# Performance work log

Hardware: AMD Instinct MI355X
Metric: run time of the kernel (lower is better)

Reference implementation:

```python
import jax, jax.numpy as jnp
import numpy as np

GRID = 480  # grid extent for both x and y voxel indices


def setup_inputs() -> dict:
    key = jax.random.key(0)
    k = jax.random.split(key, 8)
    B, N, FD, H1, H2, D = 4, 100000, 3, 128, 256, 64
    scale = 0.05
    pt_fea = jax.random.normal(k[0], (B, N, FD), dtype=jnp.float32)
    xy_ind = jax.random.randint(k[1], (B, N, 2), 0, GRID, dtype=jnp.int32)
    W1 = jax.random.normal(k[2], (FD, H1), dtype=jnp.float32) * scale
    b1 = jnp.zeros((H1,), dtype=jnp.float32)
    W2 = jax.random.normal(k[3], (H1, H2), dtype=jnp.float32) * scale
    b2 = jnp.zeros((H2,), dtype=jnp.float32)
    W3 = jax.random.normal(k[4], (H2, D), dtype=jnp.float32) * scale
    b3 = jnp.zeros((D,), dtype=jnp.float32)
    return {"pt_fea": pt_fea, "xy_ind": xy_ind, "W1": W1, "b1": b1,
            "W2": W2, "b2": b2, "W3": W3, "b3": b3}


def reference(pt_fea, xy_ind, W1, b1, W2, b2, W3, b3):
    B, N, FD = pt_fea.shape
    flat = pt_fea.reshape(B * N, FD)
    # pad xy_ind with batch id -> (b, x, y) per point
    bidx = jnp.repeat(jnp.arange(B, dtype=xy_ind.dtype), N)
    xy = xy_ind.reshape(B * N, 2)
    # lexicographic linear encoding so sorted linear order == torch.unique(dim=0) row order
    lin = (bidx.astype(jnp.int32) * GRID + xy[:, 0]) * GRID + xy[:, 1]
    unq_lin, unq_inv = jnp.unique(lin, return_inverse=True)
    M = int(unq_lin.shape[0])  # concrete: indices are concrete (eager unique)
    unq = jnp.stack([unq_lin // (GRID * GRID),
                     (unq_lin // GRID) % GRID,
                     unq_lin % GRID], axis=1)
    # per-point MLP: 3 -> 128 -> 256 -> 64
    h = jax.nn.relu(flat @ W1 + b1)
    h = jax.nn.relu(h @ W2 + b2)
    feat = h @ W3 + b3
    # scatter_max pooling per unique voxel
    pooled = jax.ops.segment_max(feat, unq_inv.reshape(-1), num_segments=M)
    return unq, pooled
```

## Files before the change

### kernel.cpp

```cpp
#include <hip/hip_runtime.h>
#include <hip/hip_bf16.h>

#define GRIDW 480
#define CELLS_PER_B (GRIDW*GRIDW)
#define NCELL (4*CELLS_PER_B)
#define NPTS  400000
#define NPB   100000
#define H1D 128
#define H2D 256
#define DD 64
#define SCAN_BLK 900
#define GRIDP 512
#define NSUB  25000
#define NWAVES (GRIDP*4)
#define CNT_NB 1563
#define EMIT_NB 3600

typedef unsigned short u16;
typedef __attribute__((ext_vector_type(8))) short bf16x8;
typedef __attribute__((ext_vector_type(4))) float f32x4;
typedef __attribute__((ext_vector_type(4))) unsigned u32x4;
typedef __attribute__((ext_vector_type(2))) unsigned u32x2;

static __device__ __forceinline__ u16 f2bf(float f){
  unsigned u = __float_as_uint(f);
  unsigned r = u + 0x7FFFu + ((u>>16)&1u);
  return (u16)(r>>16);
}
static __device__ __forceinline__ float bf2f(u16 b){
  return __uint_as_float(((unsigned)b) << 16);
}
static __device__ __forceinline__ unsigned cvt_pk_bf16(float lo, float hi){
  unsigned r;
  asm("v_cvt_pk_bf16_f32 %0, %1, %2" : "=v"(r) : "v"(lo), "v"(hi));
  return r;
}

static __device__ __forceinline__ void pack_one(int e, const float* W2, const float* W3,
                                                u16* bp2, u16* bp3){
  if (e < 32768){
    int j = e & 7, c = (e>>3)&15, ko = (e>>7)&15, n = e>>11;
    bp2[e] = f2bf(W2[(ko*8+j)*H2D + n*16 + c]);
  } else {
    int e3 = e - 32768;
    int j = e3 & 7, c = (e3>>3)&15, ko = (e3>>7)&31, n = e3>>12;
    bp3[e3] = f2bf(W3[(ko*8+j)*DD + n*16 + c]);
  }
}

__global__ void k_countpack(const int* __restrict__ xy, unsigned* __restrict__ counts,
                            const float* __restrict__ W2, const float* __restrict__ W3,
                            u16* __restrict__ bp2, u16* __restrict__ bp3){
  int b = blockIdx.x;
  if (b < CNT_NB){
    int p = b*256 + threadIdx.x;
    if (p < NPTS){
      int bb = p / NPB;
      int x = xy[2*p], y = xy[2*p+1];
      atomicAdd(&counts[(bb*GRIDW + x)*GRIDW + y], 1u);
    }
  } else {
    int e = (b - CNT_NB)*256 + threadIdx.x;
    if (e < 49152) pack_one(e, W2, W3, bp2, bp3);
  }
}

__global__ void k_scan2(const unsigned* __restrict__ counts,
                        unsigned* __restrict__ rankF, unsigned* __restrict__ rankC,
                        unsigned* __restrict__ bsumF, unsigned* __restrict__ bsumC){
  __shared__ unsigned shF[256], shC[256];
  int tid = threadIdx.x;
  int base = blockIdx.x*1024 + tid*4;
  unsigned c0=counts[base], c1=counts[base+1], c2=counts[base+2], c3=counts[base+3];
  unsigned f0=c0?1u:0u, f1=c1?1u:0u, f2=c2?1u:0u, f3=c3?1u:0u;
  unsigned sF=f0+f1+f2+f3, sC=c0+c1+c2+c3;
  shF[tid]=sF; shC[tid]=sC; __syncthreads();
  for (int off=1; off<256; off<<=1){
    unsigned tF = (tid>=off) ? shF[tid-off] : 0u;
    unsigned tC = (tid>=off) ? shC[tid-off] : 0u;
    __syncthreads();
    shF[tid] += tF; shC[tid] += tC;
    __syncthreads();
  }
  unsigned eF = shF[tid]-sF, eC = shC[tid]-sC;
  if (tid==255){ bsumF[blockIdx.x]=shF[255]; bsumC[blockIdx.x]=shC[255]; }
  rankF[base]=eF; rankF[base+1]=eF+f0; rankF[base+2]=eF+f0+f1; rankF[base+3]=eF+f0+f1+f2;
  rankC[base]=eC; rankC[base+1]=eC+c0; rankC[base+2]=eC+c0+c1; rankC[base+3]=eC+c0+c1+c2;
}

__global__ void k_scan_bsum2(unsigned* __restrict__ bsumF, unsigned* __restrict__ bsumC){
  __shared__ unsigned shF[1024], shC[1024];
  int tid = threadIdx.x;
  unsigned vF = (tid<SCAN_BLK) ? bsumF[tid] : 0u;
  unsigned vC = (tid<SCAN_BLK) ? bsumC[tid] : 0u;
  shF[tid]=vF; shC[tid]=vC; __syncthreads();
  for (int off=1; off<1024; off<<=1){
    unsigned tF = (tid>=off) ? shF[tid-off] : 0u;
    unsigned tC = (tid>=off) ? shC[tid-off] : 0u;
    __syncthreads();
    shF[tid] += tF; shC[tid] += tC;
    __syncthreads();
  }
  if (tid<SCAN_BLK){ bsumF[tid]=shF[tid]-vF; bsumC[tid]=shC[tid]-vC; }
}

__global__ void k_emitscatter(
    const unsigned* __restrict__ counts,
    const unsigned* __restrict__ rankF, unsigned* __restrict__ rankC,
    const unsigned* __restrict__ bsumF, const unsigned* __restrict__ bsumC,
    const int* __restrict__ xy,
    unsigned* __restrict__ perm, unsigned* __restrict__ vox,
    float* __restrict__ out){
  int b = blockIdx.x;
  if (b < EMIT_NB){
    int i = b*256 + threadIdx.x;
    if (counts[i]){
      unsigned rF = rankF[i] + bsumF[i>>10];
      int bb = i / CELLS_PER_B;
      int rem = i - bb*CELLS_PER_B;
      int x = rem / GRIDW;
      int y = rem - x*GRIDW;
      float* o = out + 3u*rF;
      o[0]=(float)bb; o[1]=(float)x; o[2]=(float)y;
    }
  } else {
    int p = (b - EMIT_NB)*256 + threadIdx.x;
    if (p < NPTS){
      int bb = p / NPB;
      int x = xy[2*p], y = xy[2*p+1];
      int cell = (bb*GRIDW+x)*GRIDW + y;
      unsigned slot = atomicAdd(&rankC[cell], 1u) + bsumC[cell>>10];
      perm[slot] = (unsigned)p;
      vox[slot]  = rankF[cell] + bsumF[cell>>10];
    }
  }
}

__global__ __launch_bounds__(256,2) void k_mlpp(
    const float* __restrict__ pt, const unsigned* __restrict__ perm,
    const unsigned* __restrict__ vox,
    const u16* __restrict__ bp2, const u16* __restrict__ bp3,
    const float* __restrict__ W1, const float* __restrict__ b1,
    const float* __restrict__ b2, const float* __restrict__ b3,
    float* __restrict__ outp,
    unsigned* __restrict__ pvf, unsigned* __restrict__ pvl,
    u16* __restrict__ pmf, u16* __restrict__ pml)
{
  __shared__ __attribute__((aligned(16))) u16 w2s[32768];
  __shared__ __attribute__((aligned(16))) float cf[832];
  __shared__ __attribute__((aligned(16))) u16 h2p[4][1024];

  const int tid  = threadIdx.x;
  const int lane = tid & 63;
  const int w    = tid >> 6;
  const int g    = lane >> 4;
  const int p    = lane & 15;

  for (int i = tid; i < 4096; i += 256)
    *(u32x4*)((char*)w2s + i*16) = *(const u32x4*)((const char*)bp2 + i*16);
  for (int i = tid; i < 832; i += 256){
    float v;
    if (i < 384) v = W1[i];
    else if (i < 512) v = b1[i-384];
    else if (i < 768) v = b2[i-512];
    else v = b3[i-768];
    cf[i] = v;
  }
  __syncthreads();

  u16* hb = h2p[w];

  const int wid = blockIdx.x*4 + w;
  int st = wid;

  float pf0=0.f, pf1=0.f, pf2=0.f; unsigned vx=0, pmN=0;
  if (lane < 16 && st < NSUB){
    unsigned pm0 = perm[(size_t)st*16 + lane];
    const float* q = pt + 3*(size_t)pm0;
    pf0 = q[0]; pf1 = q[1]; pf2 = q[2];
    vx = vox[(size_t)st*16 + lane];
    if (st + NWAVES < NSUB) pmN = perm[(size_t)(st+NWAVES)*16 + lane];
  }

  for (; st < NSUB; st += NWAVES){
    float nf0=0.f, nf1=0.f, nf2=0.f; unsigned nvx=0, pmN2=0;
    if (lane < 16 && st + NWAVES < NSUB){
      const float* q = pt + 3*(size_t)pmN;
      nf0 = q[0]; nf1 = q[1]; nf2 = q[2];
      nvx = vox[(size_t)(st+NWAVES)*16 + lane];
      if (st + 2*NWAVES < NSUB) pmN2 = perm[(size_t)(st+2*NWAVES)*16 + lane];
    }

    float x0 = __shfl(pf0, p, 64);
    float x1 = __shfl(pf1, p, 64);
    float x2 = __shfl(pf2, p, 64);

    bf16x8 hf[4];
    #pragma unroll
    for (int t=0;t<4;++t){
      int cb = t*32 + g*8;
      f32x4 wa0 = *(const f32x4*)&cf[cb];
      f32x4 wa1 = *(const f32x4*)&cf[cb+4];
      f32x4 wb0 = *(const f32x4*)&cf[128+cb];
      f32x4 wb1 = *(const f32x4*)&cf[128+cb+4];
      f32x4 wc0 = *(const f32x4*)&cf[256+cb];
      f32x4 wc1 = *(const f32x4*)&cf[256+cb+4];
      f32x4 a0  = *(const f32x4*)&cf[384+cb];
      f32x4 a1  = *(const f32x4*)&cf[384+cb+4];
      #pragma unroll
      for (int i=0;i<4;++i){
        a0[i] = fmaf(x0, wa0[i], a0[i]);
        a1[i] = fmaf(x0, wa1[i], a1[i]);
        a0[i] = fmaf(x1, wb0[i], a0[i]);
        a1[i] = fmaf(x1, wb1[i], a1[i]);
        a0[i] = fmaf(x2, wc0[i], a0[i]);
        a1[i] = fmaf(x2, wc1[i], a1[i]);
        a0[i] = fmaxf(a0[i], 0.f);
        a1[i] = fmaxf(a1[i], 0.f);
      }
      u32x4 ov;
      ov[0] = cvt_pk_bf16(a0[0], a0[1]);
      ov[1] = cvt_pk_bf16(a0[2], a0[3]);
      ov[2] = cvt_pk_bf16(a1[0], a1[1]);
      ov[3] = cvt_pk_bf16(a1[2], a1[3]);
      hf[t] = *(bf16x8*)&ov;
    }

    f32x4 acc3[4];
    #pragma unroll
    for (int a=0;a<4;++a){ acc3[a][0]=0.f; acc3[a][1]=0.f; acc3[a][2]=0.f; acc3[a][3]=0.f; }

    #pragma unroll
    for (int c=0;c<4;++c){
      f32x4 acc2[4];
      #pragma unroll
      for (int a=0;a<4;++a){ acc2[a][0]=0.f; acc2[a][1]=0.f; acc2[a][2]=0.f; acc2[a][3]=0.f; }
      #pragma unroll
      for (int t=0;t<4;++t){
        #pragma unroll
        for (int nn=0;nn<4;++nn){
          int ngl = c*4 + nn;
          bf16x8 w2f = *(const bf16x8*)((const char*)w2s +
                          (((ngl*16 + t*4 + g)*16) + p)*16);
          acc2[nn] = __builtin_amdgcn_mfma_f32_16x16x32_bf16(w2f, hf[t], acc2[nn], 0, 0, 0);
        }
      }
      #pragma unroll
      for (int nn=0;nn<4;++nn){
        f32x4 b2v = *(const f32x4*)&cf[512 + c*64 + nn*16 + g*4];
        float e0 = fmaxf(acc2[nn][0] + b2v[0], 0.f);
        float e1 = fmaxf(acc2[nn][1] + b2v[1], 0.f);
        float e2 = fmaxf(acc2[nn][2] + b2v[2], 0.f);
        float e3 = fmaxf(acc2[nn][3] + b2v[3], 0.f);
        u32x2 o2; o2[0] = cvt_pk_bf16(e0, e1); o2[1] = cvt_pk_bf16(e2, e3);
        unsigned byte = (unsigned)p*128u + (unsigned)(nn*32 + g*8);
        byte ^= (unsigned)(p&7) << 4;
        *(u32x2*)((char*)hb + byte) = o2;
      }
      #pragma unroll
      for (int t2=0;t2<2;++t2){
        int s = c*2 + t2;
        unsigned hbyte = (unsigned)p*128u + (unsigned)(t2*64 + g*16);
        hbyte ^= (unsigned)(p&7) << 4;
        bf16x8 h2f = *(const bf16x8*)((const char*)hb + hbyte);
        #pragma unroll
        for (int dt=0;dt<4;++dt){
          bf16x8 w3f = *(const bf16x8*)(bp3 + (((dt*32 + s*4 + g)*16) + p)*8);
          acc3[dt] = __builtin_amdgcn_mfma_f32_16x16x32_bf16(w3f, h2f, acc3[dt], 0, 0, 0);
        }
      }
    }

    #pragma unroll
    for (int dt=0;dt<4;++dt){
      f32x4 b3v = *(const f32x4*)&cf[768 + dt*16 + g*4];
      float e0 = acc3[dt][0] + b3v[0];
      float e1 = acc3[dt][1] + b3v[1];
      float e2 = acc3[dt][2] + b3v[2];
      float e3 = acc3[dt][3] + b3v[3];
      u32x2 o2; o2[0] = cvt_pk_bf16(e0, e1); o2[1] = cvt_pk_bf16(e2, e3);
      unsigned byte = (unsigned)p*128u + (unsigned)(dt*32 + g*8);
      byte ^= (unsigned)(p&7) << 4;
      *(u32x2*)((char*)hb + byte) = o2;
    }

    {
      float val[16]; unsigned vid[16];
      #pragma unroll
      for (int r=0;r<16;++r){
        unsigned byte = (unsigned)r*128u + (unsigned)lane*2u;
        byte ^= (unsigned)(r&7) << 4;
        val[r] = bf2f(*(const u16*)((const char*)hb + byte));
        vid[r] = __shfl(vx, r, 64);
      }
      float m = val[0];
      unsigned vprev = vid[0];
      int runstart = 0;
      #pragma unroll
      for (int r=1;r<16;++r){
        if (vid[r] != vprev){
          if (runstart == 0){
            pmf[(size_t)st*64 + lane] = (u16)(__float_as_uint(m)>>16);
            if (lane==0) pvf[st] = vprev;
          } else {
            outp[(size_t)vprev*64 + lane] = m;
          }
          m = val[r]; runstart = r; vprev = vid[r];
        } else m = fmaxf(m, val[r]);
      }
      pml[(size_t)st*64 + lane] = (u16)(__float_as_uint(m)>>16);
      if (lane==0) pvl[st] = vprev;
      if (runstart == 0){
        pmf[(size_t)st*64 + lane] = (u16)(__float_as_uint(m)>>16);
        if (lane==0) pvf[st] = vprev;
      }
    }
    pf0=nf0; pf1=nf1; pf2=nf2; vx=nvx; pmN=pmN2;
  }
}

__global__ __launch_bounds__(256) void k_fixup(
    const unsigned* __restrict__ pvf, const unsigned* __restrict__ pvl,
    const u16* __restrict__ pmf, const u16* __restrict__ pml,
    float* __restrict__ outp){
  int t  = blockIdx.x*4 + (threadIdx.x>>6);
  int ch = threadIdx.x & 63;
  if (t >= NSUB) return;
  unsigned vf = pvf[t], vl = pvl[t];
  if (t == 0 || pvl[t-1] != vf){
    float m = bf2f(pmf[(size_t)t*64 + ch]);
    if (vl == vf){
      m = fmaxf(m, bf2f(pml[(size_t)t*64 + ch]));
      int k = t+1;
      while (k < NSUB && pvf[k] == vf){
        m = fmaxf(m, bf2f(pmf[(size_t)k*64 + ch]));
        if (pvl[k] != vf) break;
        m = fmaxf(m, bf2f(pml[(size_t)k*64 + ch]));
        ++k;
      }
    }
    outp[(size_t)vf*64 + ch] = m;
  }
  if (vl != vf){
    float m = bf2f(pml[(size_t)t*64 + ch]);
    int k = t+1;
    while (k < NSUB && pvf[k] == vl){
      m = fmaxf(m, bf2f(pmf[(size_t)k*64 + ch]));
      if (pvl[k] != vl) break;
      m = fmaxf(m, bf2f(pml[(size_t)k*64 + ch]));
      ++k;
    }
    outp[(size_t)vl*64 + ch] = m;
  }
}

extern "C" void kernel_launch(void* const* d_in, const int* in_sizes, int n_in,
                              void* d_out, int out_size, void* d_ws, size_t ws_size,
                              hipStream_t stream){
  const float* pt = (const float*)d_in[0];
  const int*   xy = (const int*)d_in[1];
  const float* W1 = (const float*)d_in[2];
  const float* b1 = (const float*)d_in[3];
  const float* W2 = (const float*)d_in[4];
  const float* b2 = (const float*)d_in[5];
  const float* W3 = (const float*)d_in[6];
  const float* b3 = (const float*)d_in[7];
  float* out = (float*)d_out;

  int M = out_size / 67;
  float* outp = out + 3*(size_t)M;

  unsigned* counts = (unsigned*)d_ws;
  unsigned* rankF  = counts + NCELL;
  unsigned* rankC  = rankF + NCELL;
  unsigned* bsumF  = rankC + NCELL;
  unsigned* bsumC  = bsumF + 1024;
  unsigned* perm   = bsumC + 1024;
  unsigned* vox    = perm + NPTS;
  unsigned* pvf    = vox + NPTS;
  unsigned* pvl    = pvf + NSUB;
  u16* bp2 = (u16*)(pvl + NSUB);
  u16* bp3 = bp2 + 32768;
  u16* pmf = bp3 + 16384;
  u16* pml = pmf + (size_t)NSUB*64;

  hipMemsetAsync(counts, 0, NCELL*sizeof(unsigned), stream);
  k_countpack  <<<CNT_NB+192, 256, 0, stream>>>(xy, counts, W2, W3, bp2, bp3);
  k_scan2      <<<SCAN_BLK, 256, 0, stream>>>(counts, rankF, rankC, bsumF, bsumC);
  k_scan_bsum2 <<<1, 1024, 0, stream>>>(bsumF, bsumC);
  k_emitscatter<<<EMIT_NB+CNT_NB, 256, 0, stream>>>(counts, rankF, rankC, bsumF, bsumC,
                                                    xy, perm, vox, out);
  k_mlpp       <<<GRIDP, 256, 0, stream>>>(pt, perm, vox, bp2, bp3, W1, b1, b2, b3,
                                           outp, pvf, pvl, pmf, pml);
  k_fixup      <<<NSUB/4, 256, 0, stream>>>(pvf, pvl, pmf, pml, outp);
}
```

Baseline: 145.5 us.

## Fold block-sum scan into last scan block; run MLP with 16-wave blocks

```diff
diff --git a/kernel.cpp b/kernel.cpp
--- a/kernel.cpp
+++ b/kernel.cpp
@@ -10,9 +10,10 @@
 #define H2D 256
 #define DD 64
 #define SCAN_BLK 900
-#define GRIDP 512
+#define GRIDP 256
+#define WPB   16
 #define NSUB  25000
-#define NWAVES (GRIDP*4)
+#define NWAVES (GRIDP*WPB)
 #define CNT_NB 1563
 #define EMIT_NB 3600
 
@@ -67,8 +68,10 @@
 
 __global__ void k_scan2(const unsigned* __restrict__ counts,
                         unsigned* __restrict__ rankF, unsigned* __restrict__ rankC,
-                        unsigned* __restrict__ bsumF, unsigned* __restrict__ bsumC){
+                        unsigned* __restrict__ bsumF, unsigned* __restrict__ bsumC,
+                        unsigned* __restrict__ donecnt){
   __shared__ unsigned shF[256], shC[256];
+  __shared__ unsigned isLast;
   int tid = threadIdx.x;
   int base = blockIdx.x*1024 + tid*4;
   unsigned c0=counts[base], c1=counts[base+1], c2=counts[base+2], c3=counts[base+3];
@@ -86,22 +89,44 @@
   if (tid==255){ bsumF[blockIdx.x]=shF[255]; bsumC[blockIdx.x]=shC[255]; }
   rankF[base]=eF; rankF[base+1]=eF+f0; rankF[base+2]=eF+f0+f1; rankF[base+3]=eF+f0+f1+f2;
   rankC[base]=eC; rankC[base+1]=eC+c0; rankC[base+2]=eC+c0+c1; rankC[base+3]=eC+c0+c1+c2;
-}
-
-__global__ void k_scan_bsum2(unsigned* __restrict__ bsumF, unsigned* __restrict__ bsumC){
-  __shared__ unsigned shF[1024], shC[1024];
-  int tid = threadIdx.x;
-  unsigned vF = (tid<SCAN_BLK) ? bsumF[tid] : 0u;
-  unsigned vC = (tid<SCAN_BLK) ? bsumC[tid] : 0u;
-  shF[tid]=vF; shC[tid]=vC; __syncthreads();
-  for (int off=1; off<1024; off<<=1){
-    unsigned tF = (tid>=off) ? shF[tid-off] : 0u;
-    unsigned tC = (tid>=off) ? shC[tid-off] : 0u;
+
+  __threadfence();
+  __syncthreads();
+  if (tid==0){
+    unsigned old = atomicAdd(donecnt, 1u);
+    isLast = (old == SCAN_BLK-1) ? 1u : 0u;
+  }
+  __syncthreads();
+  if (isLast){
+    __threadfence();
+    volatile unsigned* vF = (volatile unsigned*)bsumF;
+    volatile unsigned* vC = (volatile unsigned*)bsumC;
+    unsigned fv[4], cv[4];
+    int b4 = tid*4;
+    #pragma unroll
+    for (int j=0;j<4;++j){
+      fv[j] = (b4+j < SCAN_BLK) ? vF[b4+j] : 0u;
+      cv[j] = (b4+j < SCAN_BLK) ? vC[b4+j] : 0u;
+    }
+    unsigned tsF = fv[0]+fv[1]+fv[2]+fv[3], tsC = cv[0]+cv[1]+cv[2]+cv[3];
     __syncthreads();
-    shF[tid] += tF; shC[tid] += tC;
-    __syncthreads();
-  }
-  if (tid<SCAN_BLK){ bsumF[tid]=shF[tid]-vF; bsumC[tid]=shC[tid]-vC; }
+    shF[tid]=tsF; shC[tid]=tsC; __syncthreads();
+    for (int off=1; off<256; off<<=1){
+      unsigned tF = (tid>=off) ? shF[tid-off] : 0u;
+      unsigned tC = (tid>=off) ? shC[tid-off] : 0u;
+      __syncthreads();
+      shF[tid] += tF; shC[tid] += tC;
+      __syncthreads();
+    }
+    unsigned pF = shF[tid]-tsF, pC = shC[tid]-tsC;
+    #pragma unroll
+    for (int j=0;j<4;++j){
+      if (b4+j < SCAN_BLK){
+        bsumF[b4+j] = pF; pF += fv[j];
+        bsumC[b4+j] = pC; pC += cv[j];
+      }
+    }
+  }
 }
 
 __global__ void k_emitscatter(
@@ -136,7 +161,7 @@
   }
 }
 
-__global__ __launch_bounds__(256,2) void k_mlpp(
+__global__ __launch_bounds__(1024,4) void k_mlpp(
     const float* __restrict__ pt, const unsigned* __restrict__ perm,
     const unsigned* __restrict__ vox,
     const u16* __restrict__ bp2, const u16* __restrict__ bp3,
@@ -148,7 +173,7 @@
 {
   __shared__ __attribute__((aligned(16))) u16 w2s[32768];
   __shared__ __attribute__((aligned(16))) float cf[832];
-  __shared__ __attribute__((aligned(16))) u16 h2p[4][1024];
+  __shared__ __attribute__((aligned(16))) u16 h2p[WPB][1024];
 
   const int tid  = threadIdx.x;
   const int lane = tid & 63;
@@ -156,9 +181,10 @@
   const int g    = lane >> 4;
   const int p    = lane & 15;
 
-  for (int i = tid; i < 4096; i += 256)
+  for (int i = tid; i < 4096; i += 1024)
     *(u32x4*)((char*)w2s + i*16) = *(const u32x4*)((const char*)bp2 + i*16);
-  for (int i = tid; i < 832; i += 256){
+  if (tid < 832){
+    int i = tid;
     float v;
     if (i < 384) v = W1[i];
     else if (i < 512) v = b1[i-384];
@@ -170,7 +196,7 @@
 
   u16* hb = h2p[w];
 
-  const int wid = blockIdx.x*4 + w;
+  const int wid = blockIdx.x*WPB + w;
   int st = wid;
 
   float pf0=0.f, pf1=0.f, pf2=0.f; unsigned vx=0, pmN=0;
@@ -370,27 +396,27 @@
   int M = out_size / 67;
   float* outp = out + 3*(size_t)M;
 
-  unsigned* counts = (unsigned*)d_ws;
-  unsigned* rankF  = counts + NCELL;
-  unsigned* rankC  = rankF + NCELL;
-  unsigned* bsumF  = rankC + NCELL;
-  unsigned* bsumC  = bsumF + 1024;
-  unsigned* perm   = bsumC + 1024;
-  unsigned* vox    = perm + NPTS;
-  unsigned* pvf    = vox + NPTS;
-  unsigned* pvl    = pvf + NSUB;
+  unsigned* counts  = (unsigned*)d_ws;
+  unsigned* donecnt = counts + NCELL;
+  unsigned* rankF   = donecnt + 1;
+  unsigned* rankC   = rankF + NCELL;
+  unsigned* bsumF   = rankC + NCELL;
+  unsigned* bsumC   = bsumF + 1024;
+  unsigned* perm    = bsumC + 1024;
+  unsigned* vox     = perm + NPTS;
+  unsigned* pvf     = vox + NPTS;
+  unsigned* pvl     = pvf + NSUB;
   u16* bp2 = (u16*)(pvl + NSUB);
   u16* bp3 = bp2 + 32768;
   u16* pmf = bp3 + 16384;
   u16* pml = pmf + (size_t)NSUB*64;
 
-  hipMemsetAsync(counts, 0, NCELL*sizeof(unsigned), stream);
+  hipMemsetAsync(counts, 0, (NCELL+1)*sizeof(unsigned), stream);
   k_countpack  <<<CNT_NB+192, 256, 0, stream>>>(xy, counts, W2, W3, bp2, bp3);
-  k_scan2      <<<SCAN_BLK, 256, 0, stream>>>(counts, rankF, rankC, bsumF, bsumC);
-  k_scan_bsum2 <<<1, 1024, 0, stream>>>(bsumF, bsumC);
+  k_scan2      <<<SCAN_BLK, 256, 0, stream>>>(counts, rankF, rankC, bsumF, bsumC, donecnt);
   k_emitscatter<<<EMIT_NB+CNT_NB, 256, 0, stream>>>(counts, rankF, rankC, bsumF, bsumC,
                                                     xy, perm, vox, out);
-  k_mlpp       <<<GRIDP, 256, 0, stream>>>(pt, perm, vox, bp2, bp3, W1, b1, b2, b3,
-                                           outp, pvf, pvl, pmf, pml);
+  k_mlpp       <<<GRIDP, 1024, 0, stream>>>(pt, perm, vox, bp2, bp3, W1, b1, b2, b3,
+                                            outp, pvf, pvl, pmf, pml);
   k_fixup      <<<NSUB/4, 256, 0, stream>>>(pvf, pvl, pmf, pml, outp);
 }
```

Measured after the change: 262.5 us. 80.4% more time.
